# Performance work log

Hardware: AMD Instinct MI355X
Metric: run time of the kernel (lower is better)

The kernel has to match this reference:

```python
import jax, jax.numpy as jnp
import numpy as np

# Production-scale M3GNet graph batch: 500 crystals, 50k atoms, 1.2M bonds, 2M triples
A, E, T, G = 50000, 1200000, 2000000, 500
U, MAXN, RBF, NTYPES, NBLOCKS = 64, 3, 48, 94, 3  # RBF = max_n*(max_l+1)^2 = 3*16


def setup_inputs() -> dict:
    key = jax.random.key(0)
    ks = jax.random.split(key, 24)

    def nrm(i, shape, s=1.0):
        return jax.random.normal(ks[i], shape, dtype=jnp.float32) * np.float32(s)

    return {
        "atom_types": jax.random.randint(ks[0], (A,), 0, NTYPES),
        "bond_atom_indices": jax.random.randint(ks[1], (E, 2), 0, A),
        "triple_bond_indices": jax.random.randint(ks[2], (T, 2), 0, E),
        "batch_atom": jnp.sort(jax.random.randint(ks[3], (A,), 0, G)),
        "bond_rbf": nrm(4, (E, MAXN)),
        "three_basis": nrm(5, (T, RBF), 0.5),
        "emb": nrm(6, (NTYPES, U), 0.5),
        "bond_W": nrm(7, (MAXN, U), 1.0 / np.sqrt(MAXN)), "bond_b": jnp.zeros((U,), jnp.float32),
        "tu_W": nrm(8, (NBLOCKS, U, RBF), 1.0 / np.sqrt(U)), "tu_b": jnp.zeros((NBLOCKS, RBF), jnp.float32),
        "tf_W1": nrm(9, (NBLOCKS, RBF, U), 1.0 / np.sqrt(RBF)), "tf_b1": jnp.zeros((NBLOCKS, U), jnp.float32),
        "tf_W2": nrm(10, (NBLOCKS, RBF, U), 1.0 / np.sqrt(RBF)), "tf_b2": jnp.zeros((NBLOCKS, U), jnp.float32),
        "gb_W1": nrm(11, (NBLOCKS, 3 * U, U), 1.0 / np.sqrt(3 * U)), "gb_b1": jnp.zeros((NBLOCKS, U), jnp.float32),
        "gb_W2": nrm(12, (NBLOCKS, 3 * U, U), 1.0 / np.sqrt(3 * U)), "gb_b2": jnp.zeros((NBLOCKS, U), jnp.float32),
        "ga_W1": nrm(13, (NBLOCKS, U, U), 1.0 / np.sqrt(U)), "ga_b1": jnp.zeros((NBLOCKS, U), jnp.float32),
        "ga_W2": nrm(14, (NBLOCKS, U, U), 1.0 / np.sqrt(U)), "ga_b2": jnp.zeros((NBLOCKS, U), jnp.float32),
        "wr_W": nrm(15, (U, U), 1.0 / np.sqrt(U)), "wr_b": jnp.zeros((U,), jnp.float32),
        "f_W1": nrm(16, (U, U), 1.0 / np.sqrt(U)), "f_b1": jnp.zeros((U,), jnp.float32),
        "f_W2": nrm(17, (U, 1), 1.0 / np.sqrt(U)), "f_b2": jnp.zeros((1,), jnp.float32),
    }


def _m3gnet(atom_types, bond_atom_indices, triple_bond_indices, batch_atom,
            bond_rbf, three_basis, emb, bond_W, bond_b, tu_W, tu_b,
            tf_W1, tf_b1, tf_W2, tf_b2, gb_W1, gb_b1, gb_W2, gb_b2,
            ga_W1, ga_b1, ga_W2, ga_b2, wr_W, wr_b, f_W1, f_b1, f_W2, f_b2):
    seg = jax.ops.segment_sum
    silu, sig = jax.nn.silu, jax.nn.sigmoid
    n_atoms, n_bonds = atom_types.shape[0], bond_rbf.shape[0]

    atom = emb[atom_types]                                # [A,U] embedding featurizer
    bond = silu(bond_rbf @ bond_W + bond_b)               # [E,U] bond_projection MLP
    src, dst = bond_atom_indices[:, 0], bond_atom_indices[:, 1]
    tb0, tb1 = triple_bond_indices[:, 0], triple_bond_indices[:, 1]
    end_atom = dst[tb1]                                   # end atom of second bond in each triple

    for i in range(NBLOCKS):
        # --- ThreeDInteraction: atom-gated three-body basis scattered onto bonds ---
        w = sig(atom @ tu_W[i] + tu_b[i])[end_atom]       # [T,RBF] update_network + gather
        agg = seg(three_basis * w, tb0, num_segments=n_bonds)  # [E,RBF]
        bond = bond + silu(agg @ tf_W1[i] + tf_b1[i]) * sig(agg @ tf_W2[i] + tf_b2[i])  # GatedMLP fusion
        # --- GraphNetworkLayer bond update (ConcatAtoms, gated, residual) ---
        cat = jnp.concatenate([atom[src], atom[dst], bond], axis=-1)  # [E,3U]
        bond = bond + silu(cat @ gb_W1[i] + gb_b1[i]) * sig(cat @ gb_W2[i] + gb_b2[i])
        # --- GraphNetworkLayer atom update (GatedAtomUpdate: gated bond msgs scattered to atoms) ---
        msg = silu(bond @ ga_W1[i] + ga_b1[i]) * sig(bond @ ga_W2[i] + ga_b2[i])
        atom = atom + seg(msg, dst, num_segments=n_atoms)

    # --- WeightedReadout (intensive): sigmoid-gated segment mean over atoms per graph ---
    gate = sig(atom @ wr_W + wr_b)
    num = seg(gate * atom, batch_atom, num_segments=G)
    cnt = seg(jnp.ones((n_atoms, 1), atom.dtype), batch_atom, num_segments=G)
    vec = num / jnp.maximum(cnt, 1.0)
    out = silu(vec @ f_W1 + f_b1) @ f_W2 + f_b2           # final MLP [units,units,1]
    return out  # [G,1]; std=1, mean=0, BaseAtomRef offset=0


def reference(atom_types, bond_atom_indices, triple_bond_indices, batch_atom,
              bond_rbf, three_basis, emb, bond_W, bond_b, tu_W, tu_b,
              tf_W1, tf_b1, tf_W2, tf_b2, gb_W1, gb_b1, gb_W2, gb_b2,
              ga_W1, ga_b1, ga_W2, ga_b2, wr_W, wr_b, f_W1, f_b1, f_W2, f_b2):
    return _m3gnet(atom_types, bond_atom_indices, triple_bond_indices, batch_atom,
                   bond_rbf, three_basis, emb, bond_W, bond_b, tu_W, tu_b,
                   tf_W1, tf_b1, tf_W2, tf_b2, gb_W1, gb_b1, gb_W2, gb_b2,
                   ga_W1, ga_b1, ga_W2, ga_b2, wr_W, wr_b, f_W1, f_b1, f_W2, f_b2)
```

## Files before the change

kernel.cpp:

```cpp
#include <hip/hip_runtime.h>
#include <cstdint>

#define A_N 50000
#define E_N 1200000
#define T_N 2000000
#define G_N 500
#define U_N 64
#define RBF_N 48
#define NB 3

#define SCAN_CHUNK 2048
#define TRI_CHUNKS ((E_N + SCAN_CHUNK - 1) / SCAN_CHUNK)
#define ATM_CHUNKS ((A_N + SCAN_CHUNK - 1) / SCAN_CHUNK)

__device__ __forceinline__ float sigf(float x){ return 1.0f/(1.0f+__expf(-x)); }
__device__ __forceinline__ float siluf(float x){ return x/(1.0f+__expf(-x)); }

__device__ __forceinline__ int sw(int k, int e){ return k*64 + (e ^ (k & 31)); }

__global__ void k_atom_init(const int* __restrict__ types, const float* __restrict__ emb,
                            float* __restrict__ atom){
  int idx = blockIdx.x*256 + threadIdx.x;
  int a = idx >> 6, u = idx & 63;
  atom[idx] = emb[types[a]*U_N + u];
}

__global__ void k_bond_init(const float* __restrict__ rbf, const float* __restrict__ bW,
                            const float* __restrict__ bb, float* __restrict__ bond){
  int idx = blockIdx.x*256 + threadIdx.x;
  int e = idx >> 6, u = idx & 63;
  float acc = bb[u];
  acc += rbf[e*3+0]*bW[0*U_N+u];
  acc += rbf[e*3+1]*bW[1*U_N+u];
  acc += rbf[e*3+2]*bW[2*U_N+u];
  bond[idx] = siluf(acc);
}


__global__ void k_scan1(const int* __restrict__ in, int* __restrict__ out,
                        int* __restrict__ sums, int n){
  __shared__ int sdata[256];
  int base = blockIdx.x*SCAN_CHUNK;
  int tid = threadIdx.x;
  int v[8]; int s = 0;
  #pragma unroll
  for (int k=0;k<8;++k){ int i = base + tid*8 + k; v[k] = (i<n) ? in[i] : 0; s += v[k]; }
  sdata[tid] = s; __syncthreads();
  #pragma unroll
  for (int off=1; off<256; off<<=1){
    int t = (tid>=off) ? sdata[tid-off] : 0;
    __syncthreads();
    sdata[tid] += t;
    __syncthreads();
  }
  int run = (tid==0) ? 0 : sdata[tid-1];
  if (tid==255) sums[blockIdx.x] = sdata[255];
  #pragma unroll
  for (int k=0;k<8;++k){ int i = base + tid*8 + k; if (i<n) out[i] = run; run += v[k]; }
}

__global__ void k_scan2(int* __restrict__ sums, int nchunks, int* __restrict__ total){
  if (blockIdx.x==0 && threadIdx.x==0){
    int acc = 0;
    for (int c=0;c<nchunks;++c){ int v = sums[c]; sums[c] = acc; acc += v; }
    *total = acc;
  }
}

__global__ void k_scan3(int* __restrict__ out, const int* __restrict__ sums, int n){
  int i = blockIdx.x*256 + threadIdx.x;
  if (i < n) out[i] += sums[i / SCAN_CHUNK];
}

__global__ void k_hist_tri(const int* __restrict__ tbi, int* __restrict__ hist){
  int t = blockIdx.x*256 + threadIdx.x;
  if (t < T_N) atomicAdd(&hist[tbi[2*t]], 1);
}

__global__ void k_scatter_tri(const int* __restrict__ tbi, const int* __restrict__ bai,
                              const int* __restrict__ offs, int* __restrict__ cursor,
                              int* __restrict__ perm, int* __restrict__ ends){
  int t = blockIdx.x*256 + threadIdx.x;
  if (t < T_N){
    int b = tbi[2*t];
    int pos = offs[b] + atomicAdd(&cursor[b], 1);
    perm[pos] = t;
    ends[pos] = bai[2*tbi[2*t+1]+1];
  }
}

__global__ void k_hist_e(const int* __restrict__ bai, int* __restrict__ hist){
  int e = blockIdx.x*256 + threadIdx.x;
  if (e < E_N) atomicAdd(&hist[bai[2*e+1]], 1);
}

__global__ void k_scatter_e(const int* __restrict__ bai, const int* __restrict__ offs,
                            int* __restrict__ cursor, int* __restrict__ eidx){
  int e = blockIdx.x*256 + threadIdx.x;
  if (e < E_N){
    int d = bai[2*e+1];
    int pos = offs[d] + atomicAdd(&cursor[d], 1);
    eidx[pos] = e;
  }
}

__global__ void k_triple_s(const float* __restrict__ tb, const int* __restrict__ perm,
                           const int* __restrict__ ends, const float* __restrict__ tuo,
                           const int* __restrict__ offs, float* __restrict__ agg){
  int idx = blockIdx.x*256 + threadIdx.x;
  int e = idx / 12, q = idx - e*12;
  int j0 = offs[e], j1 = offs[e+1];
  float4 acc = make_float4(0.f,0.f,0.f,0.f);
  for (int j=j0; j<j1; ++j){
    int t  = perm[j];
    int ea = ends[j];
    float4 b = *(const float4*)(tb  + (size_t)t *48 + q*4);
    float4 w = *(const float4*)(tuo + (size_t)ea*48 + q*4);
    acc.x = fmaf(b.x, w.x, acc.x);
    acc.y = fmaf(b.y, w.y, acc.y);
    acc.z = fmaf(b.z, w.z, acc.z);
    acc.w = fmaf(b.w, w.w, acc.w);
  }
  *(float4*)(agg + (size_t)e*48 + q*4) = acc;
}

__global__ void k_tu(const float* __restrict__ atom, const float* __restrict__ tuW,
                     const float* __restrict__ tub, float* __restrict__ tuo){
  int idx = blockIdx.x*256 + threadIdx.x;
  int a = idx / 48, r = idx - a*48;
  const float* ar = atom + a*U_N;
  float acc = tub[r];
  #pragma unroll
  for (int v=0; v<U_N; ++v) acc += ar[v]*tuW[v*48+r];
  tuo[idx] = sigf(acc);
}

__device__ __forceinline__ void accum8(const float* __restrict__ W1, const float* __restrict__ W2,
                                       int kb, int ub, const float (&c)[8],
                                       float (&acc1)[32], float (&acc2)[32]){
  #pragma unroll
  for (int k=0;k<8;++k){
    const float cv = c[k];
    const float* w1 = W1 + (size_t)(kb+k)*64 + ub;
    const float* w2 = W2 + (size_t)(kb+k)*64 + ub;
    #pragma unroll
    for (int u=0;u<32;++u){
      acc1[u] = fmaf(cv, w1[u], acc1[u]);
      acc2[u] = fmaf(cv, w2[u], acc2[u]);
    }
  }
}

__global__ __launch_bounds__(128) void k_edge(
    const float* __restrict__ agg, float* __restrict__ bond,
    const float* __restrict__ atomc, float* __restrict__ msgbuf,
    const int* __restrict__ bai,
    const float* __restrict__ tfW1, const float* __restrict__ tfb1,
    const float* __restrict__ tfW2, const float* __restrict__ tfb2,
    const float* __restrict__ gbW1, const float* __restrict__ gbb1,
    const float* __restrict__ gbW2, const float* __restrict__ gbb2,
    const float* __restrict__ gaW1, const float* __restrict__ gab1,
    const float* __restrict__ gaW2, const float* __restrict__ gab2)
{
  __shared__ float s_all[2*64*64];
  const int lane  = threadIdx.x & 63;
  const int w     = threadIdx.x >> 6;
  float* sb = s_all + w*4096;
  const int ebase = blockIdx.x*128 + w*64;
  const int e     = ebase + lane;

  #pragma unroll 1
  for (int i=0;i<64;++i)
    sb[sw(lane, i)] = bond[(size_t)(ebase+i)*64 + lane];

  const float* aggr = agg + (size_t)e*48;

  #pragma unroll 1
  for (int ug=0; ug<2; ++ug){
    const int ub = ug*32;
    float acc1[32], acc2[32];
    #pragma unroll
    for (int u=0;u<32;++u){ acc1[u] = tfb1[ub+u]; acc2[u] = tfb2[ub+u]; }
    #pragma unroll 1
    for (int kc=0;kc<6;++kc){
      float c[8];
      const float4* p = (const float4*)(aggr + kc*8);
      float4 v0 = p[0], v1 = p[1];
      c[0]=v0.x;c[1]=v0.y;c[2]=v0.z;c[3]=v0.w;c[4]=v1.x;c[5]=v1.y;c[6]=v1.z;c[7]=v1.w;
      accum8(tfW1, tfW2, kc*8, ub, c, acc1, acc2);
    }
    #pragma unroll
    for (int u=0;u<32;++u)
      sb[sw(ub+u, lane)] += siluf(acc1[u])*sigf(acc2[u]);
  }

  const int src = bai[2*e], dst = bai[2*e+1];
  const float* srow = atomc + (size_t)src*64;
  const float* drow = atomc + (size_t)dst*64;
  float res0[32];
  #pragma unroll
  for (int ug=0; ug<2; ++ug){
    const int ub = ug*32;
    float acc1[32], acc2[32];
    #pragma unroll
    for (int u=0;u<32;++u){ acc1[u] = gbb1[ub+u]; acc2[u] = gbb2[ub+u]; }
    #pragma unroll 1
    for (int s=0;s<2;++s){
      const float* row = s ? drow : srow;
      const int kb = s*64;
      #pragma unroll 1
      for (int kc=0;kc<8;++kc){
        float c[8];
        const float4* p = (const float4*)(row + kc*8);
        float4 v0 = p[0], v1 = p[1];
        c[0]=v0.x;c[1]=v0.y;c[2]=v0.z;c[3]=v0.w;c[4]=v1.x;c[5]=v1.y;c[6]=v1.z;c[7]=v1.w;
        accum8(gbW1, gbW2, kb+kc*8, ub, c, acc1, acc2);
      }
    }
    #pragma unroll 1
    for (int kc=0;kc<8;++kc){
      float c[8];
      #pragma unroll
      for (int j=0;j<8;++j) c[j] = sb[sw(kc*8+j, lane)];
      accum8(gbW1, gbW2, 128+kc*8, ub, c, acc1, acc2);
    }
    if (ug==0){
      #pragma unroll
      for (int u=0;u<32;++u)
        res0[u] = sb[sw(u, lane)] + siluf(acc1[u])*sigf(acc2[u]);
    } else {
      #pragma unroll
      for (int u=0;u<32;++u)
        sb[sw(32+u, lane)] += siluf(acc1[u])*sigf(acc2[u]);
      #pragma unroll
      for (int u=0;u<32;++u)
        sb[sw(u, lane)] = res0[u];
    }
  }

  float* mrow = msgbuf + (size_t)e*64;
  #pragma unroll 1
  for (int ug=0; ug<2; ++ug){
    const int ub = ug*32;
    float acc1[32], acc2[32];
    #pragma unroll
    for (int u=0;u<32;++u){ acc1[u] = gab1[ub+u]; acc2[u] = gab2[ub+u]; }
    #pragma unroll 1
    for (int kc=0;kc<8;++kc){
      float c[8];
      #pragma unroll
      for (int j=0;j<8;++j) c[j] = sb[sw(kc*8+j, lane)];
      accum8(gaW1, gaW2, kc*8, ub, c, acc1, acc2);
    }
    #pragma unroll
    for (int u4=0;u4<8;++u4){
      float4 mv;
      mv.x = siluf(acc1[u4*4+0])*sigf(acc2[u4*4+0]);
      mv.y = siluf(acc1[u4*4+1])*sigf(acc2[u4*4+1]);
      mv.z = siluf(acc1[u4*4+2])*sigf(acc2[u4*4+2]);
      mv.w = siluf(acc1[u4*4+3])*sigf(acc2[u4*4+3]);
      *(float4*)(mrow + ub + u4*4) = mv;
    }
  }

  #pragma unroll 1
  for (int i=0;i<64;++i)
    bond[(size_t)(ebase+i)*64 + lane] = sb[sw(lane, i)];
}

__global__ void k_msg_agg(const float* __restrict__ msgbuf, const int* __restrict__ eidx,
                          const int* __restrict__ offs, const float* __restrict__ atomc,
                          float* __restrict__ atomn){
  int idx = blockIdx.x*256 + threadIdx.x;
  int a = idx >> 6, u = idx & 63;
  int j0 = offs[a], j1 = offs[a+1];
  float s = atomc[idx];
  for (int j=j0; j<j1; ++j)
    s += msgbuf[(size_t)eidx[j]*64 + u];
  atomn[idx] = s;
}

__global__ void k_gate(const float* __restrict__ atom, const int* __restrict__ batch,
                       const float* __restrict__ wrW, const float* __restrict__ wrb,
                       float* __restrict__ num, float* __restrict__ cnt){
  int idx = blockIdx.x*256 + threadIdx.x;
  int a = idx >> 6, u = idx & 63;
  const float* ar = atom + (size_t)a*64;
  float acc = wrb[u];
  #pragma unroll
  for (int v=0;v<64;++v) acc += ar[v]*wrW[v*64+u];
  float g = sigf(acc);
  int b = batch[a];
  atomicAdd(&num[b*64+u], g*ar[u]);
  if (u==0) atomicAdd(&cnt[b], 1.0f);
}

__global__ __launch_bounds__(64) void k_final(const float* __restrict__ num, const float* __restrict__ cnt,
                        const float* __restrict__ fW1, const float* __restrict__ fb1,
                        const float* __restrict__ fW2, const float* __restrict__ fb2,
                        float* __restrict__ out){
  int g = blockIdx.x; int u = threadIdx.x;
  float inv = 1.0f / fmaxf(cnt[g], 1.0f);
  float acc = fb1[u];
  #pragma unroll
  for (int v=0;v<64;++v) acc += num[g*64+v]*inv*fW1[v*64+u];
  float p = siluf(acc)*fW2[u];
  #pragma unroll
  for (int off=32; off>0; off>>=1) p += __shfl_down(p, off, 64);
  if (u==0) out[g] = p + fb2[0];
}

extern "C" void kernel_launch(void* const* d_in, const int* in_sizes, int n_in,
                              void* d_out, int out_size, void* d_ws, size_t ws_size,
                              hipStream_t stream){
  const int*   atom_types = (const int*)d_in[0];
  const int*   bai   = (const int*)d_in[1];
  const int*   tbi   = (const int*)d_in[2];
  const int*   batch = (const int*)d_in[3];
  const float* rbf   = (const float*)d_in[4];
  const float* tb    = (const float*)d_in[5];
  const float* emb   = (const float*)d_in[6];
  const float* bW    = (const float*)d_in[7];
  const float* bb    = (const float*)d_in[8];
  const float* tuW   = (const float*)d_in[9];
  const float* tub   = (const float*)d_in[10];
  const float* tfW1  = (const float*)d_in[11];
  const float* tfb1  = (const float*)d_in[12];
  const float* tfW2  = (const float*)d_in[13];
  const float* tfb2  = (const float*)d_in[14];
  const float* gbW1  = (const float*)d_in[15];
  const float* gbb1  = (const float*)d_in[16];
  const float* gbW2  = (const float*)d_in[17];
  const float* gbb2  = (const float*)d_in[18];
  const float* gaW1  = (const float*)d_in[19];
  const float* gab1  = (const float*)d_in[20];
  const float* gaW2  = (const float*)d_in[21];
  const float* gab2  = (const float*)d_in[22];
  const float* wrW   = (const float*)d_in[23];
  const float* wrb   = (const float*)d_in[24];
  const float* fW1   = (const float*)d_in[25];
  const float* fb1   = (const float*)d_in[26];
  const float* fW2   = (const float*)d_in[27];
  const float* fb2   = (const float*)d_in[28];

  char* ws = (char*)d_ws;
  size_t off = 0;
  auto alloc = [&](size_t bytes)->char* {
    char* p = ws + off; off += (bytes + 255) & ~size_t(255); return p;
  };
  float* bond    = (float*)alloc((size_t)E_N*64*4);
  float* agg     = (float*)alloc((size_t)E_N*48*4);
  float* msgbuf  = (float*)alloc((size_t)E_N*64*4);
  float* atomA   = (float*)alloc((size_t)A_N*64*4);
  float* atomB   = (float*)alloc((size_t)A_N*64*4);
  float* tuo     = (float*)alloc((size_t)A_N*48*4);
  float* num     = (float*)alloc((size_t)G_N*64*4);
  float* cnt     = (float*)alloc((size_t)G_N*4);
  int*   tri_offs= (int*)  alloc((size_t)(E_N+1)*4);
  int*   tri_hist= (int*)  alloc((size_t)E_N*4);
  int*   tri_perm= (int*)  alloc((size_t)T_N*4);
  int*   tri_ends= (int*)  alloc((size_t)T_N*4);
  int*   e_offs  = (int*)  alloc((size_t)(A_N+1)*4);
  int*   e_hist  = (int*)  alloc((size_t)A_N*4);
  int*   e_idx   = (int*)  alloc((size_t)E_N*4);
  int*   scan_sums=(int*)  alloc(4096);

  k_atom_init<<<A_N*64/256, 256, 0, stream>>>(atom_types, emb, atomA);
  k_bond_init<<<E_N*64/256, 256, 0, stream>>>(rbf, bW, bb, bond);

  hipMemsetAsync(tri_hist, 0, (size_t)E_N*4, stream);
  k_hist_tri<<<(T_N+255)/256, 256, 0, stream>>>(tbi, tri_hist);
  k_scan1<<<TRI_CHUNKS, 256, 0, stream>>>(tri_hist, tri_offs, scan_sums, E_N);
  k_scan2<<<1, 64, 0, stream>>>(scan_sums, TRI_CHUNKS, tri_offs + E_N);
  k_scan3<<<(E_N+255)/256, 256, 0, stream>>>(tri_offs, scan_sums, E_N);
  hipMemsetAsync(tri_hist, 0, (size_t)E_N*4, stream);
  k_scatter_tri<<<(T_N+255)/256, 256, 0, stream>>>(tbi, bai, tri_offs, tri_hist,
                                                   tri_perm, tri_ends);

  hipMemsetAsync(e_hist, 0, (size_t)A_N*4, stream);
  k_hist_e<<<(E_N+255)/256, 256, 0, stream>>>(bai, e_hist);
  k_scan1<<<ATM_CHUNKS, 256, 0, stream>>>(e_hist, e_offs, scan_sums, A_N);
  k_scan2<<<1, 64, 0, stream>>>(scan_sums, ATM_CHUNKS, e_offs + A_N);
  k_scan3<<<(A_N+255)/256, 256, 0, stream>>>(e_offs, scan_sums, A_N);
  hipMemsetAsync(e_hist, 0, (size_t)A_N*4, stream);
  k_scatter_e<<<(E_N+255)/256, 256, 0, stream>>>(bai, e_offs, e_hist, e_idx);

  hipMemsetAsync(num, 0, G_N*64*4, stream);
  hipMemsetAsync(cnt, 0, G_N*4, stream);

  float* cur = atomA; float* nxt = atomB;
  for (int i=0;i<NB;++i){
    k_tu<<<A_N*48/256, 256, 0, stream>>>(cur, tuW + (size_t)i*64*48, tub + (size_t)i*48, tuo);
    k_triple_s<<<E_N*12/256, 256, 0, stream>>>(tb, tri_perm, tri_ends, tuo, tri_offs, agg);
    k_edge<<<E_N/128, 128, 0, stream>>>(agg, bond, cur, msgbuf, bai,
        tfW1 + (size_t)i*48*64, tfb1 + (size_t)i*64,
        tfW2 + (size_t)i*48*64, tfb2 + (size_t)i*64,
        gbW1 + (size_t)i*192*64, gbb1 + (size_t)i*64,
        gbW2 + (size_t)i*192*64, gbb2 + (size_t)i*64,
        gaW1 + (size_t)i*64*64, gab1 + (size_t)i*64,
        gaW2 + (size_t)i*64*64, gab2 + (size_t)i*64);
    k_msg_agg<<<A_N*64/256, 256, 0, stream>>>(msgbuf, e_idx, e_offs, cur, nxt);
    float* t2 = cur; cur = nxt; nxt = t2;
  }
  k_gate<<<A_N*64/256, 256, 0, stream>>>(cur, batch, wrW, wrb, num, cnt);
  k_final<<<G_N, 64, 0, stream>>>(num, cnt, fW1, fb1, fW2, fb2, (float*)d_out);
}
```

Measured before the change: 10.50 ms.

## Keep per-edge bond row in registers instead of swizzled shared memory

The edge kernel no longer stages each edge's 64-float bond row in a swizzled LDS tile. It holds the row in registers, loaded and stored with float4 row-wise accesses instead of coalesced column transposes. The gated bond MLP is split into four 16-wide output chunks with a stash so register pressure stays bounded, and launch bounds request three blocks per SM. This removes LDS traffic and the transpose loops, but raises VGPR usage and may cause spills. Per-thread row-wise global accesses are also less coalesced than the old lane-per-column pattern, and the shared weight loads are now repeated per chunk.

Result: slower. 11.00 ms (+4.7%).

```diff
diff --git a/kernel.cpp b/kernel.cpp
--- a/kernel.cpp
+++ b/kernel.cpp
@@ -15,8 +15,6 @@
 
 __device__ __forceinline__ float sigf(float x){ return 1.0f/(1.0f+__expf(-x)); }
 __device__ __forceinline__ float siluf(float x){ return x/(1.0f+__expf(-x)); }
-
-__device__ __forceinline__ int sw(int k, int e){ return k*64 + (e ^ (k & 31)); }
 
 __global__ void k_atom_init(const int* __restrict__ types, const float* __restrict__ emb,
                             float* __restrict__ atom){
@@ -151,7 +149,23 @@
   }
 }
 
-__global__ __launch_bounds__(128) void k_edge(
+__device__ __forceinline__ void accum16(const float* __restrict__ W1, const float* __restrict__ W2,
+                                        int kb, int ub, const float (&c)[8],
+                                        float (&acc1)[16], float (&acc2)[16]){
+  #pragma unroll
+  for (int k=0;k<8;++k){
+    const float cv = c[k];
+    const float* w1 = W1 + (size_t)(kb+k)*64 + ub;
+    const float* w2 = W2 + (size_t)(kb+k)*64 + ub;
+    #pragma unroll
+    for (int u=0;u<16;++u){
+      acc1[u] = fmaf(cv, w1[u], acc1[u]);
+      acc2[u] = fmaf(cv, w2[u], acc2[u]);
+    }
+  }
+}
+
+__global__ __launch_bounds__(128, 3) void k_edge(
     const float* __restrict__ agg, float* __restrict__ bond,
     const float* __restrict__ atomc, float* __restrict__ msgbuf,
     const int* __restrict__ bai,
@@ -162,20 +176,21 @@
     const float* __restrict__ gaW1, const float* __restrict__ gab1,
     const float* __restrict__ gaW2, const float* __restrict__ gab2)
 {
-  __shared__ float s_all[2*64*64];
-  const int lane  = threadIdx.x & 63;
-  const int w     = threadIdx.x >> 6;
-  float* sb = s_all + w*4096;
-  const int ebase = blockIdx.x*128 + w*64;
-  const int e     = ebase + lane;
-
-  #pragma unroll 1
-  for (int i=0;i<64;++i)
-    sb[sw(lane, i)] = bond[(size_t)(ebase+i)*64 + lane];
+  const int e = blockIdx.x*128 + threadIdx.x;
+
+  float b[64];
+  {
+    const float* brow = bond + (size_t)e*64;
+    #pragma unroll
+    for (int q=0;q<16;++q){
+      float4 v = *(const float4*)(brow + q*4);
+      b[q*4+0]=v.x; b[q*4+1]=v.y; b[q*4+2]=v.z; b[q*4+3]=v.w;
+    }
+  }
 
   const float* aggr = agg + (size_t)e*48;
 
-  #pragma unroll 1
+  #pragma unroll
   for (int ug=0; ug<2; ++ug){
     const int ub = ug*32;
     float acc1[32], acc2[32];
@@ -191,66 +206,74 @@
     }
     #pragma unroll
     for (int u=0;u<32;++u)
-      sb[sw(ub+u, lane)] += siluf(acc1[u])*sigf(acc2[u]);
+      b[ub+u] += siluf(acc1[u])*sigf(acc2[u]);
   }
 
   const int src = bai[2*e], dst = bai[2*e+1];
   const float* srow = atomc + (size_t)src*64;
   const float* drow = atomc + (size_t)dst*64;
-  float res0[32];
+  float stash[48];
+  #pragma unroll
+  for (int ch=0; ch<4; ++ch){
+    const int ub = ch*16;
+    float acc1[16], acc2[16];
+    #pragma unroll
+    for (int u=0;u<16;++u){ acc1[u] = gbb1[ub+u]; acc2[u] = gbb2[ub+u]; }
+    #pragma unroll 1
+    for (int kc=0;kc<8;++kc){
+      float c[8];
+      const float4* p = (const float4*)(srow + kc*8);
+      float4 v0 = p[0], v1 = p[1];
+      c[0]=v0.x;c[1]=v0.y;c[2]=v0.z;c[3]=v0.w;c[4]=v1.x;c[5]=v1.y;c[6]=v1.z;c[7]=v1.w;
+      accum16(gbW1, gbW2, kc*8, ub, c, acc1, acc2);
+    }
+    #pragma unroll 1
+    for (int kc=0;kc<8;++kc){
+      float c[8];
+      const float4* p = (const float4*)(drow + kc*8);
+      float4 v0 = p[0], v1 = p[1];
+      c[0]=v0.x;c[1]=v0.y;c[2]=v0.z;c[3]=v0.w;c[4]=v1.x;c[5]=v1.y;c[6]=v1.z;c[7]=v1.w;
+      accum16(gbW1, gbW2, 64+kc*8, ub, c, acc1, acc2);
+    }
+    #pragma unroll
+    for (int k=0;k<64;++k){
+      const float cv = b[k];
+      const float* w1 = gbW1 + (size_t)(128+k)*64 + ub;
+      const float* w2 = gbW2 + (size_t)(128+k)*64 + ub;
+      #pragma unroll
+      for (int u=0;u<16;++u){
+        acc1[u] = fmaf(cv, w1[u], acc1[u]);
+        acc2[u] = fmaf(cv, w2[u], acc2[u]);
+      }
+    }
+    if (ch < 3){
+      #pragma unroll
+      for (int u=0;u<16;++u) stash[ch*16+u] = siluf(acc1[u])*sigf(acc2[u]);
+    } else {
+      #pragma unroll
+      for (int u=0;u<16;++u) b[48+u] += siluf(acc1[u])*sigf(acc2[u]);
+      #pragma unroll
+      for (int j=0;j<48;++j) b[j] += stash[j];
+    }
+  }
+
+  float* mrow = msgbuf + (size_t)e*64;
   #pragma unroll
   for (int ug=0; ug<2; ++ug){
     const int ub = ug*32;
     float acc1[32], acc2[32];
     #pragma unroll
-    for (int u=0;u<32;++u){ acc1[u] = gbb1[ub+u]; acc2[u] = gbb2[ub+u]; }
-    #pragma unroll 1
-    for (int s=0;s<2;++s){
-      const float* row = s ? drow : srow;
-      const int kb = s*64;
-      #pragma unroll 1
-      for (int kc=0;kc<8;++kc){
-        float c[8];
-        const float4* p = (const float4*)(row + kc*8);
-        float4 v0 = p[0], v1 = p[1];
-        c[0]=v0.x;c[1]=v0.y;c[2]=v0.z;c[3]=v0.w;c[4]=v1.x;c[5]=v1.y;c[6]=v1.z;c[7]=v1.w;
-        accum8(gbW1, gbW2, kb+kc*8, ub, c, acc1, acc2);
+    for (int u=0;u<32;++u){ acc1[u] = gab1[ub+u]; acc2[u] = gab2[ub+u]; }
+    #pragma unroll
+    for (int k=0;k<64;++k){
+      const float cv = b[k];
+      const float* w1 = gaW1 + (size_t)k*64 + ub;
+      const float* w2 = gaW2 + (size_t)k*64 + ub;
+      #pragma unroll
+      for (int u=0;u<32;++u){
+        acc1[u] = fmaf(cv, w1[u], acc1[u]);
+        acc2[u] = fmaf(cv, w2[u], acc2[u]);
       }
-    }
-    #pragma unroll 1
-    for (int kc=0;kc<8;++kc){
-      float c[8];
-      #pragma unroll
-      for (int j=0;j<8;++j) c[j] = sb[sw(kc*8+j, lane)];
-      accum8(gbW1, gbW2, 128+kc*8, ub, c, acc1, acc2);
-    }
-    if (ug==0){
-      #pragma unroll
-      for (int u=0;u<32;++u)
-        res0[u] = sb[sw(u, lane)] + siluf(acc1[u])*sigf(acc2[u]);
-    } else {
-      #pragma unroll
-      for (int u=0;u<32;++u)
-        sb[sw(32+u, lane)] += siluf(acc1[u])*sigf(acc2[u]);
-      #pragma unroll
-      for (int u=0;u<32;++u)
-        sb[sw(u, lane)] = res0[u];
-    }
-  }
-
-  float* mrow = msgbuf + (size_t)e*64;
-  #pragma unroll 1
-  for (int ug=0; ug<2; ++ug){
-    const int ub = ug*32;
-    float acc1[32], acc2[32];
-    #pragma unroll
-    for (int u=0;u<32;++u){ acc1[u] = gab1[ub+u]; acc2[u] = gab2[ub+u]; }
-    #pragma unroll 1
-    for (int kc=0;kc<8;++kc){
-      float c[8];
-      #pragma unroll
-      for (int j=0;j<8;++j) c[j] = sb[sw(kc*8+j, lane)];
-      accum8(gaW1, gaW2, kc*8, ub, c, acc1, acc2);
     }
     #pragma unroll
     for (int u4=0;u4<8;++u4){
@@ -263,9 +286,15 @@
     }
   }
 
-  #pragma unroll 1
-  for (int i=0;i<64;++i)
-    bond[(size_t)(ebase+i)*64 + lane] = sb[sw(lane, i)];
+  {
+    float* brow = bond + (size_t)e*64;
+    #pragma unroll
+    for (int q=0;q<16;++q){
+      float4 v;
+      v.x=b[q*4+0]; v.y=b[q*4+1]; v.z=b[q*4+2]; v.w=b[q*4+3];
+      *(float4*)(brow + q*4) = v;
+    }
+  }
 }
 
 __global__ void k_msg_agg(const float* __restrict__ msgbuf, const int* __restrict__ eidx,
```
